# Kernel tuning notes

Hardware: AMD Instinct MI355X
Metric: run time of the kernel (lower is better)

## Reference

```python
import jax, jax.numpy as jnp
import numpy as np

S, B, D, H, A = 256, 1024, 64, 128, 8  # seq_len, buffer, state_size, hidden, action_size


def _init(key, shape, fan_in):
    bound = 1.0 / np.sqrt(fan_in)
    return jax.random.uniform(key, shape, jnp.float32, -bound, bound)


def setup_inputs() -> dict:
    key = jax.random.key(0)
    ks = jax.random.split(key, 24)
    inp = {"state": jax.random.normal(ks[0], (S, B, D), jnp.float32)}
    # actor / critic MLPs (Linear(D,H) + ReLU + Linear(H,H) + ReLU)
    inp["aw1"] = _init(ks[1], (H, D), D); inp["ab1"] = _init(ks[2], (H,), D)
    inp["aw2"] = _init(ks[3], (H, H), H); inp["ab2"] = _init(ks[4], (H,), H)
    inp["cw1"] = _init(ks[5], (H, D), D); inp["cb1"] = _init(ks[6], (H,), D)
    inp["cw2"] = _init(ks[7], (H, H), H); inp["cb2"] = _init(ks[8], (H,), H)
    # LSTMs (PyTorch layout: W_ih [4H,H], W_hh [4H,H], gate order i,f,g,o)
    inp["a_wih"] = _init(ks[9], (4 * H, H), H); inp["a_whh"] = _init(ks[10], (4 * H, H), H)
    inp["a_bih"] = _init(ks[11], (4 * H,), H); inp["a_bhh"] = _init(ks[12], (4 * H,), H)
    inp["c_wih"] = _init(ks[13], (4 * H, H), H); inp["c_whh"] = _init(ks[14], (4 * H, H), H)
    inp["c_bih"] = _init(ks[15], (4 * H,), H); inp["c_bhh"] = _init(ks[16], (4 * H,), H)
    # heads
    inp["mw"] = _init(ks[17], (A, H), H); inp["mb"] = _init(ks[18], (A,), H)
    inp["lw"] = _init(ks[19], (A, H), H); inp["lb"] = _init(ks[20], (A,), H)
    inp["vw"] = _init(ks[21], (1, H), H); inp["vb"] = _init(ks[22], (1,), H)
    return inp


def _mlp(x, w1, b1, w2, b2):
    h = jax.nn.relu(jnp.einsum('sbd,hd->sbh', x, w1) + b1)
    return jax.nn.relu(jnp.einsum('sbh,gh->sbg', h, w2) + b2)


def _lstm_zero_state(x, w_ih, b_ih, b_hh):
    # Each timestep runs with fresh zero (h, c): the recurrent term vanishes,
    # so the whole sequence is one batched GEMM + gating (W_hh unused).
    gates = jnp.einsum('sbh,gh->sbg', x, w_ih) + b_ih + b_hh  # [S,B,4H]
    i, f, g, o = jnp.split(gates, 4, axis=-1)
    c = jax.nn.sigmoid(i) * jnp.tanh(g)  # f * c_prev = 0
    return jax.nn.sigmoid(o) * jnp.tanh(c)


def reference(state, aw1, ab1, aw2, ab2, cw1, cb1, cw2, cb2,
              a_wih, a_whh, a_bih, a_bhh, c_wih, c_whh, c_bih, c_bhh,
              mw, mb, lw, lb, vw, vb):
    actor_h = _lstm_zero_state(_mlp(state, aw1, ab1, aw2, ab2), a_wih, a_bih, a_bhh)
    critic_h = _lstm_zero_state(_mlp(state, cw1, cb1, cw2, cb2), c_wih, c_bih, c_bhh)
    mean = jnp.einsum('sbh,ah->sba', actor_h, mw) + mb
    std = jnp.exp(jnp.einsum('sbh,ah->sba', actor_h, lw) + lb)
    value = jnp.einsum('sbh,vh->sbv', critic_h, vw) + vb
    return (mean, std, value)
```

## Files before the change

### kernel.cpp

```cpp
#include <hip/hip_runtime.h>


#define NROWS (256 * 1024)
#define HID 128
#define ACTD 8

#define W1_OFF 0
#define W2_OFF 16384
#define WI_OFF 49152
#define WG_OFF 81920
#define WO_OFF 114688
#define PSTR 147456
#define HEAD_OFF (2 * PSTR)
#define GB_OFF (HEAD_OFF + 8192)

#define NEG_L (-1.4426950408889634f)
#define TWO_L (2.8853900817779268f)

typedef __attribute__((ext_vector_type(8))) short s16x8;
typedef __attribute__((ext_vector_type(4))) float fx4;
typedef __attribute__((ext_vector_type(2))) unsigned int u32x2;
typedef __attribute__((ext_vector_type(4))) unsigned int u32x4;

__device__ __forceinline__ unsigned int cvtpk(float lo, float hi) {
  unsigned int r;
  asm("v_cvt_pk_bf16_f32 %0, %1, %2" : "=v"(r) : "v"(lo), "v"(hi));
  return r;
}

__device__ __forceinline__ float ex2(float x) {
  return __builtin_amdgcn_exp2f(x);
}
__device__ __forceinline__ float frcp(float x) {
  return __builtin_amdgcn_rcpf(x);
}

__device__ __forceinline__ void dma16(const void* g, void* l) {
  __builtin_amdgcn_global_load_lds(
      (__attribute__((address_space(1))) void*)(g),
      (__attribute__((address_space(3))) void*)(l), 16, 0, 0);
}

__device__ __forceinline__ s16x8 frag_ld(const unsigned short* base, int row,
                                         int kbyte, int rowsh) {
  int byte = (row << rowsh) + (kbyte ^ ((row & 7) << 4));
  return *(const s16x8*)((const char*)base + byte);
}

__device__ __forceinline__ void zacc(fx4 acc[4][2]) {
#pragma unroll
  for (int j = 0; j < 4; ++j)
#pragma unroll
    for (int i = 0; i < 2; ++i) acc[j][i] = fx4{0.f, 0.f, 0.f, 0.f};
}

template <int KC, int WSH, int ASH>
__device__ __forceinline__ void gemm_fs(const unsigned short* wt,
                                        const unsigned short* at, int wv,
                                        int lane, fx4 acc[4][2]) {
  const int l15 = lane & 15;
  const int kb0 = (lane >> 4) << 4;
#pragma unroll
  for (int kc = 0; kc < KC; ++kc) {
    int kbyte = kc * 64 + kb0;
    s16x8 w0 = frag_ld(wt, (wv * 2 + 0) * 16 + l15, kbyte, WSH);
    s16x8 w1 = frag_ld(wt, (wv * 2 + 1) * 16 + l15, kbyte, WSH);
#pragma unroll
    for (int jt = 0; jt < 4; ++jt) {
      s16x8 a = frag_ld(at, jt * 16 + l15, kbyte, ASH);
      acc[jt][0] = __builtin_amdgcn_mfma_f32_16x16x32_bf16(w0, a, acc[jt][0], 0, 0, 0);
      acc[jt][1] = __builtin_amdgcn_mfma_f32_16x16x32_bf16(w1, a, acc[jt][1], 0, 0, 0);
    }
  }
}

__device__ __forceinline__ void epi_relu(fx4 acc[4][2],
                                         const float* __restrict__ bias,
                                         unsigned short* obuf, int fb,
                                         int lane) {
  const int g4 = (lane >> 4) << 2;
  const int l15 = lane & 15;
  char* ob = (char*)obuf;
#pragma unroll
  for (int it = 0; it < 2; ++it) {
    int n0 = fb + it * 16 + g4;
    fx4 bv = *(const fx4*)(bias + n0);
#pragma unroll
    for (int jt = 0; jt < 4; ++jt) {
      fx4 v = acc[jt][it] + bv;
#pragma unroll
      for (int r = 0; r < 4; ++r) v[r] = fmaxf(v[r], 0.0f);
      u32x2 u;
      u[0] = cvtpk(v[0], v[1]);
      u[1] = cvtpk(v[2], v[3]);
      int m = jt * 16 + l15;
      *(u32x2*)(ob + (m << 8) + ((n0 * 2) ^ ((m & 7) << 4))) = u;
    }
  }
}

__global__ void prep_weights(const float* __restrict__ aw1,
                             const float* __restrict__ aw2,
                             const float* __restrict__ awih,
                             const float* __restrict__ cw1,
                             const float* __restrict__ cw2,
                             const float* __restrict__ cwih,
                             const float* __restrict__ mw,
                             const float* __restrict__ lw,
                             const float* __restrict__ vw,
                             const float* __restrict__ abih,
                             const float* __restrict__ abhh,
                             const float* __restrict__ cbih,
                             const float* __restrict__ cbhh,
                             char* __restrict__ ws) {
  int y = blockIdx.y;
  int idx = blockIdx.x * 256 + threadIdx.x;
  if (y >= 12) {
    if (idx < 384) {
      float* dst = (float*)(ws + GB_OFF + (size_t)(y - 12) * 1536);
      const float* b0 = (y == 12) ? abih : cbih;
      const float* b1 = (y == 12) ? abhh : cbhh;
      int sect = idx >> 7, f = idx & 127;
      int srow = (sect == 0) ? f : (sect == 1) ? 256 + f : 384 + f;
      float scale = (sect == 1) ? TWO_L : NEG_L;
      dst[idx] = scale * (b0[srow] + b1[srow]);
    }
    return;
  }
  if (y >= 10) {
    if (idx >= 256) return;
    int row = idx >> 4, c16 = idx & 15;
    fx4 v0 = {0.f, 0.f, 0.f, 0.f}, v1 = v0;
    if (y == 10) {
      const float* src = (row < 8) ? (mw + (size_t)row * HID + c16 * 8)
                                   : (lw + (size_t)(row - 8) * HID + c16 * 8);
      v0 = ((const fx4*)src)[0];
      v1 = ((const fx4*)src)[1];
    } else if (row == 0) {
      const float* src = vw + c16 * 8;
      v0 = ((const fx4*)src)[0];
      v1 = ((const fx4*)src)[1];
    }
    u32x4 u;
    u[0] = cvtpk(v0[0], v0[1]);
    u[1] = cvtpk(v0[2], v0[3]);
    u[2] = cvtpk(v1[0], v1[1]);
    u[3] = cvtpk(v1[2], v1[3]);
    int byte = (row << 8) + ((c16 << 4) ^ ((row & 7) << 4));
    *(u32x4*)(ws + HEAD_OFF + (size_t)(y - 10) * 4096 + byte) = u;
    return;
  }
  const float* src;
  int nch, sh, off;
  switch (y) {
    case 0:  src = aw1;              nch = 1024; sh = 3; off = W1_OFF;        break;
    case 1:  src = aw2;              nch = 2048; sh = 4; off = W2_OFF;        break;
    case 2:  src = awih;             nch = 2048; sh = 4; off = WI_OFF;        break;
    case 3:  src = awih + 256 * HID; nch = 2048; sh = 4; off = WG_OFF;        break;
    case 4:  src = awih + 384 * HID; nch = 2048; sh = 4; off = WO_OFF;        break;
    case 5:  src = cw1;              nch = 1024; sh = 3; off = PSTR + W1_OFF; break;
    case 6:  src = cw2;              nch = 2048; sh = 4; off = PSTR + W2_OFF; break;
    case 7:  src = cwih;             nch = 2048; sh = 4; off = PSTR + WI_OFF; break;
    case 8:  src = cwih + 256 * HID; nch = 2048; sh = 4; off = PSTR + WG_OFF; break;
    default: src = cwih + 384 * HID; nch = 2048; sh = 4; off = PSTR + WO_OFF; break;
  }
  if (idx >= nch) return;
  int r = idx >> sh;
  int c = idx & ((1 << sh) - 1);
  const fx4* gp = (const fx4*)(src + (size_t)idx * 8);
  fx4 v0 = gp[0], v1 = gp[1];
  u32x4 u;
  u[0] = cvtpk(v0[0], v0[1]);
  u[1] = cvtpk(v0[2], v0[3]);
  u[2] = cvtpk(v1[0], v1[1]);
  u[3] = cvtpk(v1[2], v1[3]);
  int byte = (r << (sh + 4)) + ((c << 4) ^ ((r & 7) << 4));
  *(u32x4*)(ws + off + byte) = u;
}

__global__ __launch_bounds__(256, 3) void fused_ac(
    const float* __restrict__ state, const float* __restrict__ ab1,
    const float* __restrict__ ab2, const float* __restrict__ cb1,
    const float* __restrict__ cb2, const float* __restrict__ mb,
    const float* __restrict__ lb, const float* __restrict__ vb,
    const char* __restrict__ ws, float* __restrict__ outp) {
  __shared__ __align__(16) unsigned short wbuf[16384];
  __shared__ __align__(16) unsigned short abuf[8192];

  const int tid = threadIdx.x;
  const int lane = tid & 63;
  const int wv = tid >> 6;
  const int l15 = lane & 15;
  const int g4 = (lane >> 4) << 2;
  const int kb0 = (lane >> 4) << 4;
  const int fb = wv << 5;
  const int path = blockIdx.x >> 12;
  const int rbase = (blockIdx.x & 4095) << 6;

  const char* wsp = ws + (size_t)path * PSTR;
  const float* b1 = path ? cb1 : ab1;
  const float* b2 = path ? cb2 : ab2;
  const float* gb = (const float*)(ws + GB_OFF + (size_t)path * 1536);
  char* wb = (char*)wbuf;

  float* meanp = outp;
  float* stdp = outp + (size_t)NROWS * ACTD;
  float* valp = outp + (size_t)NROWS * ACTD * 2;

#pragma unroll
  for (int i = 0; i < 4; ++i) dma16(wsp + W1_OFF + (tid + i * 256) * 16, wb + (tid + i * 256) * 16);
  {
    const float* xg = state + (size_t)rbase * 64;
#pragma unroll
    for (int i = 0; i < 2; ++i) {
      int idx = tid + i * 256;
      int r = idx >> 3, c = idx & 7;
      const fx4* gp = (const fx4*)(xg + idx * 8);
      fx4 v0 = gp[0], v1 = gp[1];
      u32x4 u;
      u[0] = cvtpk(v0[0], v0[1]);
      u[1] = cvtpk(v0[2], v0[3]);
      u[2] = cvtpk(v1[0], v1[1]);
      u[3] = cvtpk(v1[2], v1[3]);
      *(u32x4*)(wb + 16384 + r * 128 + ((c << 4) ^ ((r & 7) << 4))) = u;
    }
  }
  __syncthreads();

  fx4 acc[4][2];
  zacc(acc);
  gemm_fs<2, 7, 7>(wbuf, wbuf + 8192, wv, lane, acc);
  __syncthreads();
#pragma unroll
  for (int i = 0; i < 8; ++i) dma16(wsp + W2_OFF + (tid + i * 256) * 16, wb + (tid + i * 256) * 16);
  epi_relu(acc, b1, abuf, fb, lane);
  __syncthreads();

  zacc(acc);
  gemm_fs<4, 8, 8>(wbuf, abuf, wv, lane, acc);
  __syncthreads();
#pragma unroll
  for (int i = 0; i < 8; ++i) dma16(wsp + WI_OFF + (tid + i * 256) * 16, wb + (tid + i * 256) * 16);
  epi_relu(acc, b2, abuf, fb, lane);
  __syncthreads();

  zacc(acc);
  gemm_fs<4, 8, 8>(wbuf, abuf, wv, lane, acc);
  __syncthreads();
#pragma unroll
  for (int i = 0; i < 8; ++i) dma16(wsp + WG_OFF + (tid + i * 256) * 16, wb + (tid + i * 256) * 16);
  fx4 carry[4][2];
#pragma unroll
  for (int it = 0; it < 2; ++it) {
    fx4 pv = *(const fx4*)(gb + fb + it * 16 + g4);
#pragma unroll
    for (int jt = 0; jt < 4; ++jt)
#pragma unroll
      for (int r = 0; r < 4; ++r)
        carry[jt][it][r] = ex2(fmaf(acc[jt][it][r], NEG_L, pv[r]));
  }
  __syncthreads();

  zacc(acc);
  gemm_fs<4, 8, 8>(wbuf, abuf, wv, lane, acc);
  __syncthreads();
#pragma unroll
  for (int i = 0; i < 8; ++i) dma16(wsp + WO_OFF + (tid + i * 256) * 16, wb + (tid + i * 256) * 16);
#pragma unroll
  for (int it = 0; it < 2; ++it) {
    fx4 pv = *(const fx4*)(gb + 128 + fb + it * 16 + g4);
#pragma unroll
    for (int jt = 0; jt < 4; ++jt)
#pragma unroll
      for (int r = 0; r < 4; ++r) {
        float Eg = ex2(fmaf(acc[jt][it][r], TWO_L, pv[r]));
        float c = (Eg - 1.0f) * frcp((Eg + 1.0f) * (carry[jt][it][r] + 1.0f));
        carry[jt][it][r] = ex2(c * TWO_L);
      }
  }
  __syncthreads();

  zacc(acc);
  gemm_fs<4, 8, 8>(wbuf, abuf, wv, lane, acc);
  __syncthreads();
  if (tid < 256) dma16(ws + HEAD_OFF + (size_t)path * 4096 + tid * 16, wb + tid * 16);
  {
    char* ob = (char*)abuf;
#pragma unroll
    for (int it = 0; it < 2; ++it) {
      fx4 pv = *(const fx4*)(gb + 256 + fb + it * 16 + g4);
      int n0 = fb + it * 16 + g4;
#pragma unroll
      for (int jt = 0; jt < 4; ++jt) {
        fx4 h;
#pragma unroll
        for (int r = 0; r < 4; ++r) {
          float Eo = ex2(fmaf(acc[jt][it][r], NEG_L, pv[r]));
          float Ec = carry[jt][it][r];
          h[r] = (Ec - 1.0f) * frcp((Ec + 1.0f) * (Eo + 1.0f));
        }
        u32x2 u;
        u[0] = cvtpk(h[0], h[1]);
        u[1] = cvtpk(h[2], h[3]);
        int m = jt * 16 + l15;
        *(u32x2*)(ob + (m << 8) + ((n0 * 2) ^ ((m & 7) << 4))) = u;
      }
    }
  }
  __syncthreads();

  fx4 ha = fx4{0.f, 0.f, 0.f, 0.f};
#pragma unroll
  for (int kc = 0; kc < 4; ++kc) {
    int kbyte = kc * 64 + kb0;
    s16x8 w = frag_ld(wbuf, l15, kbyte, 8);
    s16x8 a = frag_ld(abuf, (wv << 4) + l15, kbyte, 8);
    ha = __builtin_amdgcn_mfma_f32_16x16x32_bf16(w, a, ha, 0, 0, 0);
  }

  int m = rbase + (wv << 4) + l15;
  if (path == 0) {
    if (g4 < 8) {
      fx4 v = ha + *(const fx4*)(mb + g4);
      *(fx4*)(meanp + (size_t)m * ACTD + g4) = v;
    } else {
      fx4 v;
#pragma unroll
      for (int r = 0; r < 4; ++r) v[r] = __expf(ha[r] + lb[g4 - 8 + r]);
      *(fx4*)(stdp + (size_t)m * ACTD + (g4 - 8)) = v;
    }
  } else if (g4 == 0) {
    valp[m] = ha[0] + vb[0];
  }
}

extern "C" void kernel_launch(void* const* d_in, const int* in_sizes, int n_in,
                              void* d_out, int out_size, void* d_ws,
                              size_t ws_size, hipStream_t stream) {
  (void)in_sizes; (void)n_in; (void)ws_size; (void)out_size;
  const float* state = (const float*)d_in[0];
  const float* aw1 = (const float*)d_in[1];
  const float* ab1 = (const float*)d_in[2];
  const float* aw2 = (const float*)d_in[3];
  const float* ab2 = (const float*)d_in[4];
  const float* cw1 = (const float*)d_in[5];
  const float* cb1 = (const float*)d_in[6];
  const float* cw2 = (const float*)d_in[7];
  const float* cb2 = (const float*)d_in[8];
  const float* awih = (const float*)d_in[9];
  const float* abih = (const float*)d_in[11];
  const float* abhh = (const float*)d_in[12];
  const float* cwih = (const float*)d_in[13];
  const float* cbih = (const float*)d_in[15];
  const float* cbhh = (const float*)d_in[16];
  const float* mw = (const float*)d_in[17];
  const float* mb = (const float*)d_in[18];
  const float* lw = (const float*)d_in[19];
  const float* lb = (const float*)d_in[20];
  const float* vw = (const float*)d_in[21];
  const float* vb = (const float*)d_in[22];
  char* ws = (char*)d_ws;

  prep_weights<<<dim3(8, 14), 256, 0, stream>>>(
      aw1, aw2, awih, cw1, cw2, cwih, mw, lw, vw, abih, abhh, cbih, cbhh, ws);
  fused_ac<<<8192, 256, 0, stream>>>(state, ab1, ab2, cb1, cb2, mb, lb, vb, ws,
                                     (float*)d_out);
}
```

Measured before the change: 128.6 us.

## Load weight fragments directly from global memory in MFMA order, drop LDS weight staging

Weights are pre-packed by the prep kernel into an MFMA-fragment-contiguous layout, so each lane reads its operand fragment straight from global/L2 memory instead of staging whole weight matrices through LDS via DMA. This removes the 32KB LDS weight buffer, which allows more blocks per CU, and removes several barriers between the LSTM gate GEMMs. Biases are now folded into the accumulator initialization. The trade-off is that every wave re-reads weights from the cache hierarchy on every GEMM, relying on L1/L2 hits instead of shared LDS reuse.

```diff
diff --git a/kernel.cpp b/kernel.cpp
--- a/kernel.cpp
+++ b/kernel.cpp
@@ -35,12 +35,6 @@
   return __builtin_amdgcn_rcpf(x);
 }
 
-__device__ __forceinline__ void dma16(const void* g, void* l) {
-  __builtin_amdgcn_global_load_lds(
-      (__attribute__((address_space(1))) void*)(g),
-      (__attribute__((address_space(3))) void*)(l), 16, 0, 0);
-}
-
 __device__ __forceinline__ s16x8 frag_ld(const unsigned short* base, int row,
                                          int kbyte, int rowsh) {
   int byte = (row << rowsh) + (kbyte ^ ((row & 7) << 4));
@@ -54,17 +48,28 @@
     for (int i = 0; i < 2; ++i) acc[j][i] = fx4{0.f, 0.f, 0.f, 0.f};
 }
 
-template <int KC, int WSH, int ASH>
-__device__ __forceinline__ void gemm_fs(const unsigned short* wt,
-                                        const unsigned short* at, int wv,
-                                        int lane, fx4 acc[4][2]) {
+__device__ __forceinline__ void bacc(fx4 acc[4][2], const float* __restrict__ b,
+                                     int fb, int g4) {
+#pragma unroll
+  for (int it = 0; it < 2; ++it) {
+    fx4 bv = *(const fx4*)(b + fb + it * 16 + g4);
+#pragma unroll
+    for (int jt = 0; jt < 4; ++jt) acc[jt][it] = bv;
+  }
+}
+
+template <int KC, int ASH>
+__device__ __forceinline__ void gemm_g(const char* __restrict__ wimg,
+                                       const unsigned short* at, int wv,
+                                       int lane, fx4 acc[4][2]) {
   const int l15 = lane & 15;
   const int kb0 = (lane >> 4) << 4;
+  const int woff = ((lane >> 4) << 8) + (l15 << 4);
 #pragma unroll
   for (int kc = 0; kc < KC; ++kc) {
     int kbyte = kc * 64 + kb0;
-    s16x8 w0 = frag_ld(wt, (wv * 2 + 0) * 16 + l15, kbyte, WSH);
-    s16x8 w1 = frag_ld(wt, (wv * 2 + 1) * 16 + l15, kbyte, WSH);
+    s16x8 w0 = *(const s16x8*)(wimg + (((wv * 2 + 0) * KC + kc) << 10) + woff);
+    s16x8 w1 = *(const s16x8*)(wimg + (((wv * 2 + 1) * KC + kc) << 10) + woff);
 #pragma unroll
     for (int jt = 0; jt < 4; ++jt) {
       s16x8 a = frag_ld(at, jt * 16 + l15, kbyte, ASH);
@@ -74,20 +79,17 @@
   }
 }
 
-__device__ __forceinline__ void epi_relu(fx4 acc[4][2],
-                                         const float* __restrict__ bias,
-                                         unsigned short* obuf, int fb,
-                                         int lane) {
+__device__ __forceinline__ void epi_relu(fx4 acc[4][2], unsigned short* obuf,
+                                         int fb, int lane) {
   const int g4 = (lane >> 4) << 2;
   const int l15 = lane & 15;
   char* ob = (char*)obuf;
 #pragma unroll
   for (int it = 0; it < 2; ++it) {
     int n0 = fb + it * 16 + g4;
-    fx4 bv = *(const fx4*)(bias + n0);
 #pragma unroll
     for (int jt = 0; jt < 4; ++jt) {
-      fx4 v = acc[jt][it] + bv;
+      fx4 v = acc[jt][it];
 #pragma unroll
       for (int r = 0; r < 4; ++r) v[r] = fmaxf(v[r], 0.0f);
       u32x2 u;
@@ -129,7 +131,7 @@
   }
   if (y >= 10) {
     if (idx >= 256) return;
-    int row = idx >> 4, c16 = idx & 15;
+    int row = idx >> 4, c16 = idx & 15, kc = c16 >> 2, ks = c16 & 3;
     fx4 v0 = {0.f, 0.f, 0.f, 0.f}, v1 = v0;
     if (y == 10) {
       const float* src = (row < 8) ? (mw + (size_t)row * HID + c16 * 8)
@@ -146,27 +148,28 @@
     u[1] = cvtpk(v0[2], v0[3]);
     u[2] = cvtpk(v1[0], v1[1]);
     u[3] = cvtpk(v1[2], v1[3]);
-    int byte = (row << 8) + ((c16 << 4) ^ ((row & 7) << 4));
-    *(u32x4*)(ws + HEAD_OFF + (size_t)(y - 10) * 4096 + byte) = u;
+    int dst = ((kc * 4 + ks) * 16 + row) * 16;
+    *(u32x4*)(ws + HEAD_OFF + (size_t)(y - 10) * 4096 + dst) = u;
     return;
   }
   const float* src;
-  int nch, sh, off;
+  int nch, ksh, KC, off;
   switch (y) {
-    case 0:  src = aw1;              nch = 1024; sh = 3; off = W1_OFF;        break;
-    case 1:  src = aw2;              nch = 2048; sh = 4; off = W2_OFF;        break;
-    case 2:  src = awih;             nch = 2048; sh = 4; off = WI_OFF;        break;
-    case 3:  src = awih + 256 * HID; nch = 2048; sh = 4; off = WG_OFF;        break;
-    case 4:  src = awih + 384 * HID; nch = 2048; sh = 4; off = WO_OFF;        break;
-    case 5:  src = cw1;              nch = 1024; sh = 3; off = PSTR + W1_OFF; break;
-    case 6:  src = cw2;              nch = 2048; sh = 4; off = PSTR + W2_OFF; break;
-    case 7:  src = cwih;             nch = 2048; sh = 4; off = PSTR + WI_OFF; break;
-    case 8:  src = cwih + 256 * HID; nch = 2048; sh = 4; off = PSTR + WG_OFF; break;
-    default: src = cwih + 384 * HID; nch = 2048; sh = 4; off = PSTR + WO_OFF; break;
+    case 0:  src = aw1;              nch = 1024; ksh = 3; KC = 2; off = W1_OFF;        break;
+    case 1:  src = aw2;              nch = 2048; ksh = 4; KC = 4; off = W2_OFF;        break;
+    case 2:  src = awih;             nch = 2048; ksh = 4; KC = 4; off = WI_OFF;        break;
+    case 3:  src = awih + 256 * HID; nch = 2048; ksh = 4; KC = 4; off = WG_OFF;        break;
+    case 4:  src = awih + 384 * HID; nch = 2048; ksh = 4; KC = 4; off = WO_OFF;        break;
+    case 5:  src = cw1;              nch = 1024; ksh = 3; KC = 2; off = PSTR + W1_OFF; break;
+    case 6:  src = cw2;              nch = 2048; ksh = 4; KC = 4; off = PSTR + W2_OFF; break;
+    case 7:  src = cwih;             nch = 2048; ksh = 4; KC = 4; off = PSTR + WI_OFF; break;
+    case 8:  src = cwih + 256 * HID; nch = 2048; ksh = 4; KC = 4; off = PSTR + WG_OFF; break;
+    default: src = cwih + 384 * HID; nch = 2048; ksh = 4; KC = 4; off = PSTR + WO_OFF; break;
   }
   if (idx >= nch) return;
-  int r = idx >> sh;
-  int c = idx & ((1 << sh) - 1);
+  int row = idx >> ksh;
+  int c16 = idx & ((1 << ksh) - 1);
+  int b2 = row >> 4, r = row & 15, kc = c16 >> 2, ks = c16 & 3;
   const fx4* gp = (const fx4*)(src + (size_t)idx * 8);
   fx4 v0 = gp[0], v1 = gp[1];
   u32x4 u;
@@ -174,8 +177,8 @@
   u[1] = cvtpk(v0[2], v0[3]);
   u[2] = cvtpk(v1[0], v1[1]);
   u[3] = cvtpk(v1[2], v1[3]);
-  int byte = (r << (sh + 4)) + ((c << 4) ^ ((r & 7) << 4));
-  *(u32x4*)(ws + off + byte) = u;
+  int dst = (((b2 * KC + kc) * 4 + ks) * 16 + r) * 16;
+  *(u32x4*)(ws + off + dst) = u;
 }
 
 __global__ __launch_bounds__(256, 3) void fused_ac(
@@ -184,7 +187,6 @@
     const float* __restrict__ cb2, const float* __restrict__ mb,
     const float* __restrict__ lb, const float* __restrict__ vb,
     const char* __restrict__ ws, float* __restrict__ outp) {
-  __shared__ __align__(16) unsigned short wbuf[16384];
   __shared__ __align__(16) unsigned short abuf[8192];
 
   const int tid = threadIdx.x;
@@ -201,16 +203,15 @@
   const float* b1 = path ? cb1 : ab1;
   const float* b2 = path ? cb2 : ab2;
   const float* gb = (const float*)(ws + GB_OFF + (size_t)path * 1536);
-  char* wb = (char*)wbuf;
+  const char* himg = ws + HEAD_OFF + (size_t)path * 4096;
 
   float* meanp = outp;
   float* stdp = outp + (size_t)NROWS * ACTD;
   float* valp = outp + (size_t)NROWS * ACTD * 2;
 
-#pragma unroll
-  for (int i = 0; i < 4; ++i) dma16(wsp + W1_OFF + (tid + i * 256) * 16, wb + (tid + i * 256) * 16);
   {
     const float* xg = state + (size_t)rbase * 64;
+    char* ab = (char*)abuf;
 #pragma unroll
     for (int i = 0; i < 2; ++i) {
       int idx = tid + i * 256;
@@ -222,34 +223,27 @@
       u[1] = cvtpk(v0[2], v0[3]);
       u[2] = cvtpk(v1[0], v1[1]);
       u[3] = cvtpk(v1[2], v1[3]);
-      *(u32x4*)(wb + 16384 + r * 128 + ((c << 4) ^ ((r & 7) << 4))) = u;
+      *(u32x4*)(ab + r * 128 + ((c << 4) ^ ((r & 7) << 4))) = u;
     }
   }
   __syncthreads();
 
   fx4 acc[4][2];
+  bacc(acc, b1, fb, g4);
+  gemm_g<2, 7>(wsp + W1_OFF, abuf, wv, lane, acc);
+  __syncthreads();
+  epi_relu(acc, abuf, fb, lane);
+  __syncthreads();
+
+  bacc(acc, b2, fb, g4);
+  gemm_g<4, 8>(wsp + W2_OFF, abuf, wv, lane, acc);
+  __syncthreads();
+  epi_relu(acc, abuf, fb, lane);
+  __syncthreads();
+
+  fx4 carry[4][2];
   zacc(acc);
-  gemm_fs<2, 7, 7>(wbuf, wbuf + 8192, wv, lane, acc);
-  __syncthreads();
-#pragma unroll
-  for (int i = 0; i < 8; ++i) dma16(wsp + W2_OFF + (tid + i * 256) * 16, wb + (tid + i * 256) * 16);
-  epi_relu(acc, b1, abuf, fb, lane);
-  __syncthreads();
-
-  zacc(acc);
-  gemm_fs<4, 8, 8>(wbuf, abuf, wv, lane, acc);
-  __syncthreads();
-#pragma unroll
-  for (int i = 0; i < 8; ++i) dma16(wsp + WI_OFF + (tid + i * 256) * 16, wb + (tid + i * 256) * 16);
-  epi_relu(acc, b2, abuf, fb, lane);
-  __syncthreads();
-
-  zacc(acc);
-  gemm_fs<4, 8, 8>(wbuf, abuf, wv, lane, acc);
-  __syncthreads();
-#pragma unroll
-  for (int i = 0; i < 8; ++i) dma16(wsp + WG_OFF + (tid + i * 256) * 16, wb + (tid + i * 256) * 16);
-  fx4 carry[4][2];
+  gemm_g<4, 8>(wsp + WI_OFF, abuf, wv, lane, acc);
 #pragma unroll
   for (int it = 0; it < 2; ++it) {
     fx4 pv = *(const fx4*)(gb + fb + it * 16 + g4);
@@ -259,13 +253,9 @@
       for (int r = 0; r < 4; ++r)
         carry[jt][it][r] = ex2(fmaf(acc[jt][it][r], NEG_L, pv[r]));
   }
-  __syncthreads();
 
   zacc(acc);
-  gemm_fs<4, 8, 8>(wbuf, abuf, wv, lane, acc);
-  __syncthreads();
-#pragma unroll
-  for (int i = 0; i < 8; ++i) dma16(wsp + WO_OFF + (tid + i * 256) * 16, wb + (tid + i * 256) * 16);
+  gemm_g<4, 8>(wsp + WG_OFF, abuf, wv, lane, acc);
 #pragma unroll
   for (int it = 0; it < 2; ++it) {
     fx4 pv = *(const fx4*)(gb + 128 + fb + it * 16 + g4);
@@ -278,12 +268,10 @@
         carry[jt][it][r] = ex2(c * TWO_L);
       }
   }
-  __syncthreads();
 
   zacc(acc);
-  gemm_fs<4, 8, 8>(wbuf, abuf, wv, lane, acc);
-  __syncthreads();
-  if (tid < 256) dma16(ws + HEAD_OFF + (size_t)path * 4096 + tid * 16, wb + tid * 16);
+  gemm_g<4, 8>(wsp + WO_OFF, abuf, wv, lane, acc);
+  __syncthreads();
   {
     char* ob = (char*)abuf;
 #pragma unroll
@@ -310,11 +298,11 @@
   __syncthreads();
 
   fx4 ha = fx4{0.f, 0.f, 0.f, 0.f};
+  const int woff = ((lane >> 4) << 8) + (l15 << 4);
 #pragma unroll
   for (int kc = 0; kc < 4; ++kc) {
-    int kbyte = kc * 64 + kb0;
-    s16x8 w = frag_ld(wbuf, l15, kbyte, 8);
-    s16x8 a = frag_ld(abuf, (wv << 4) + l15, kbyte, 8);
+    s16x8 w = *(const s16x8*)(himg + (kc << 10) + woff);
+    s16x8 a = frag_ld(abuf, (wv << 4) + l15, kc * 64 + kb0, 8);
     ha = __builtin_amdgcn_mfma_f32_16x16x32_bf16(w, a, ha, 0, 0, 0);
   }
 
```

Result: faster. 125.6 us (-2.3%).
